# Kernel tuning notes

Hardware: AMD Instinct MI355X
Metric: run time of the kernel (lower is better)

## Reference

```python
import jax, jax.numpy as jnp
import numpy as np

D = 1024        # embedding_dim
H = 16          # num_heads
HKV = 4         # num_kv_heads
HD = D // H     # head_dim = 64
L = 64          # latent_dim
EPS = 1e-6
LN_EPS = 1e-5
B, S = 2, 1024


def _feat(x):
    # feature_map == 'elu': elu(x) + 1 (non-negative features)
    return jax.nn.elu(x) + 1.0


def setup_inputs() -> dict:
    key = jax.random.key(0)
    ks = jax.random.split(key, 8)
    w = lambda k, shape: (jax.random.normal(k, shape, jnp.float32) * 0.02)
    return {
        "x": jax.random.normal(ks[0], (B, S, D), jnp.float32),
        "Wq": w(ks[1], (D, D)), "bq": jnp.zeros((D,), jnp.float32),
        "Wk": w(ks[2], (D, HKV * HD)), "bk": jnp.zeros((HKV * HD,), jnp.float32),
        "Wv": w(ks[3], (D, HKV * HD)), "bv": jnp.zeros((HKV * HD,), jnp.float32),
        "Wc": w(ks[4], (HKV * HD, L)),   # kv_compress (no bias)
        "We": w(ks[5], (L, HKV * HD)),   # kv_expand (no bias)
        "Wo": w(ks[6], (D, D)), "bo": jnp.zeros((D,), jnp.float32),
        "gamma": jnp.ones((D,), jnp.float32),
        "beta": jnp.zeros((D,), jnp.float32),
    }


def reference(x, Wq, bq, Wk, bk, Wv, bv, Wc, We, Wo, bo, gamma, beta):
    b, s, _ = x.shape
    residual = x
    # projections
    q = x @ Wq + bq                     # [b,s,D]
    k = x @ Wk + bk                     # [b,s,HKV*HD]
    v = x @ Wv + bv
    # latent compress -> expand
    k = (k @ Wc) @ We                   # [b,s,HKV*HD]
    v = (v @ Wc) @ We
    # split heads
    q = q.reshape(b, s, H, HD).transpose(0, 2, 1, 3)      # [b,H,s,HD]
    k = k.reshape(b, s, HKV, HD).transpose(0, 2, 1, 3)    # [b,HKV,s,HD]
    v = v.reshape(b, s, HKV, HD).transpose(0, 2, 1, 3)
    # GQA: repeat KV heads per query group
    rep = H // HKV
    k = jnp.repeat(k, rep, axis=1)                        # [b,H,s,HD]
    v = jnp.repeat(v, rep, axis=1)
    # causal linear attention via cumulative KV outer-product state
    qf = _feat(q)                                          # [b,h,s,f]
    kf = _feat(k)
    kv = jnp.einsum('bhsf,bhsd->bhsfd', kf, v)             # [b,h,s,f,d]
    kv_cum = jnp.cumsum(kv, axis=2)
    num = jnp.einsum('bhsf,bhsfd->bhsd', qf, kv_cum)
    den = jnp.einsum('bhsf,bhsf->bhs', qf, jnp.cumsum(kf, axis=2))[..., None] + EPS
    o = num / den                                          # [b,h,s,d]
    # merge heads, output projection
    o = o.transpose(0, 2, 1, 3).reshape(b, s, D)
    o = o @ Wo + bo
    # residual + layernorm (epsilon=1e-5)
    y = residual + o
    mu = jnp.mean(y, axis=-1, keepdims=True)
    var = jnp.var(y, axis=-1, keepdims=True)
    return (y - mu) / jnp.sqrt(var + LN_EPS) * gamma + beta
```

## Files before the change

kernel.cpp:

```cpp
#include <hip/hip_runtime.h>

#define D_ 1024
#define H_ 16
#define HKV_ 4
#define B_ 2
#define S_ 1024
#define BS_ (B_*S_)
#define QKVW 1536
#define QB 64
#define NC (S_/QB)

typedef short bf8 __attribute__((ext_vector_type(8)));
typedef float f32x4 __attribute__((ext_vector_type(4)));

#define MFMA_B16(a,b,c) __builtin_amdgcn_mfma_f32_16x16x32_bf16((a),(b),(c),0,0,0)

#define GLOAD16(g, l) __builtin_amdgcn_global_load_lds( \
    (const __attribute__((address_space(1))) void*)(g), \
    (__attribute__((address_space(3))) void*)(l), 16, 0, 0)

#define SW(row, idx) ((idx) ^ (((row) & 7) << 3))

__device__ __forceinline__ unsigned short f2b(float f) {
  unsigned int u = __float_as_uint(f);
  u += 0x7FFFu + ((u >> 16) & 1u);
  return (unsigned short)(u >> 16);
}
__device__ __forceinline__ float b2f(unsigned short h) {
  return __uint_as_float(((unsigned int)h) << 16);
}
__device__ __forceinline__ float feat(float x) { return x > 0.f ? x + 1.f : __expf(x); }

__device__ __forceinline__ void conv_body(const float* __restrict__ src,
                                          unsigned short* __restrict__ dst,
                                          int sub, int n4, int tid) {
  int i = sub * 256 + tid;
  if (i >= n4) return;
  float4 v = ((const float4*)src)[i];
  ushort4 o;
  o.x = f2b(v.x); o.y = f2b(v.y); o.z = f2b(v.z); o.w = f2b(v.w);
  ((ushort4*)dst)[i] = o;
}

__device__ __forceinline__ void tconv_body(const float* __restrict__ src,
                                           unsigned short* __restrict__ dst,
                                           int bx, int by, int ss, int ds,
                                           int tid, float (*tl)[65]) {
  int r0 = by * 64, c0 = bx * 64;
  int ty = tid >> 4, tx4 = (tid & 15) * 4;
#pragma unroll
  for (int rep = 0; rep < 4; ++rep) {
    int r = ty + rep * 16;
    float4 v = *(const float4*)&src[(size_t)(r0 + r) * ss + c0 + tx4];
    tl[r][tx4] = v.x; tl[r][tx4 + 1] = v.y; tl[r][tx4 + 2] = v.z; tl[r][tx4 + 3] = v.w;
  }
  __syncthreads();
#pragma unroll
  for (int rep = 0; rep < 4; ++rep) {
    int c = ty + rep * 16;
    ushort4 o;
    o.x = f2b(tl[tx4 + 0][c]); o.y = f2b(tl[tx4 + 1][c]);
    o.z = f2b(tl[tx4 + 2][c]); o.w = f2b(tl[tx4 + 3][c]);
    *(ushort4*)&dst[(size_t)(c0 + c) * ds + r0 + tx4] = o;
  }
}

__global__ __launch_bounds__(256) void k_prep(const float* __restrict__ x,
                                              const float* __restrict__ Wq,
                                              const float* __restrict__ Wo,
                                              const float* __restrict__ Wk,
                                              const float* __restrict__ Wv,
                                              const float* __restrict__ Wc,
                                              const float* __restrict__ We,
                                              unsigned short* __restrict__ xb,
                                              unsigned short* __restrict__ Wqkv_t,
                                              unsigned short* __restrict__ Wo_t,
                                              unsigned short* __restrict__ Wkv_b,
                                              float* __restrict__ Wce,
                                              unsigned short* __restrict__ Wce_t) {
  __shared__ float tl[64][65];
  __shared__ __align__(16) unsigned short As[64][72];
  __shared__ __align__(16) unsigned short Bs[128][72];
  int blk = blockIdx.x, tid = threadIdx.x;
  if (blk < 2048) {
    conv_body(x, xb, blk, BS_ * D_ / 4, tid);
  } else if (blk < 2304) {
    conv_body(Wk, Wkv_b, blk - 2048, 1024 * 256 / 4, tid);
  } else if (blk < 2560) {
    conv_body(Wv, Wkv_b + 1024 * 256, blk - 2304, 1024 * 256 / 4, tid);
  } else if (blk < 2816) {
    int sb = blk - 2560;
    tconv_body(Wq, Wqkv_t, sb & 15, sb >> 4, 1024, 1024, tid, tl);
  } else if (blk < 3072) {
    int sb = blk - 2816;
    tconv_body(Wo, Wo_t, sb & 15, sb >> 4, 1024, 1024, tid, tl);
  } else {
    int sb = blk - 3072;
    int row0 = (sb >> 1) * 64, col0 = (sb & 1) * 128;
    {
      int r = tid >> 2, c0 = (tid & 3) * 16;
      const float* src = &Wc[(size_t)(row0 + r) * 64 + c0];
#pragma unroll
      for (int e = 0; e < 16; e += 4) {
        float4 v = *(const float4*)(src + e);
        As[r][c0 + e] = f2b(v.x); As[r][c0 + e + 1] = f2b(v.y);
        As[r][c0 + e + 2] = f2b(v.z); As[r][c0 + e + 3] = f2b(v.w);
      }
      int k = tid >> 2, cb = (tid & 3) * 32;
      const float* wsrc = &We[(size_t)k * 256 + col0 + cb];
#pragma unroll
      for (int e = 0; e < 32; e += 4) {
        float4 v = *(const float4*)(wsrc + e);
        Bs[cb + e][k] = f2b(v.x); Bs[cb + e + 1][k] = f2b(v.y);
        Bs[cb + e + 2][k] = f2b(v.z); Bs[cb + e + 3][k] = f2b(v.w);
      }
    }
    __syncthreads();
    const int lane = tid & 63, wave = tid >> 6;
    const int lr = lane & 15, lq = lane >> 4;
    const int wc0 = wave * 32;
    const f32x4 fzero = {0.f, 0.f, 0.f, 0.f};
    f32x4 acc[4][2];
#pragma unroll
    for (int i = 0; i < 4; ++i) { acc[i][0] = fzero; acc[i][1] = fzero; }
#pragma unroll
    for (int kk = 0; kk < 2; ++kk)
#pragma unroll
      for (int mi = 0; mi < 4; ++mi) {
        bf8 a = *(const bf8*)&As[mi * 16 + lr][kk * 32 + lq * 8];
#pragma unroll
        for (int ni = 0; ni < 2; ++ni) {
          bf8 bb = *(const bf8*)&Bs[wc0 + ni * 16 + lr][kk * 32 + lq * 8];
          acc[mi][ni] = MFMA_B16(a, bb, acc[mi][ni]);
        }
      }
#pragma unroll
    for (int mi = 0; mi < 4; ++mi)
#pragma unroll
      for (int ni = 0; ni < 2; ++ni) {
        int col = col0 + wc0 + ni * 16 + lr;
#pragma unroll
        for (int r = 0; r < 4; ++r) {
          int row = row0 + mi * 16 + lq * 4 + r;
          float v = acc[mi][ni][r];
          Wce[(size_t)row * 256 + col] = v;
          Wce_t[(size_t)col * 256 + row] = f2b(v);
        }
      }
  }
}

template<int MODE>
__global__ __launch_bounds__(64) void k_gemm1(const unsigned short* __restrict__ A,
                                              const unsigned short* __restrict__ Bt,
                                              const float* __restrict__ bias,
                                              unsigned short* __restrict__ C,
                                              int N, int K) {
  __shared__ __align__(16) unsigned short As[2][64 * 64];
  __shared__ __align__(16) unsigned short Bs[2][64 * 64];
  const int lane = threadIdx.x;
  const int row0 = blockIdx.y * 64, col0 = blockIdx.x * 64;
  const int lr = lane & 15, lq = lane >> 4;
  const int rsub = lane >> 3, sj = lane & 7;
  const int js = sj ^ rsub;
  const f32x4 fzero = {0.f, 0.f, 0.f, 0.f};
  f32x4 acc[4][4];
#pragma unroll
  for (int i = 0; i < 4; ++i)
#pragma unroll
    for (int j = 0; j < 4; ++j) acc[i][j] = fzero;

#define STAGE64(pb, k0)                                                        \
  {                                                                            \
    _Pragma("unroll")                                                          \
    for (int i = 0; i < 8; ++i)                                                \
      GLOAD16(&A[(size_t)(row0 + i * 8 + rsub) * K + (k0) + js * 8],           \
              &As[pb][(i * 512 + lane * 8)]);                                  \
    _Pragma("unroll")                                                          \
    for (int i = 0; i < 8; ++i)                                                \
      GLOAD16(&Bt[(size_t)(col0 + i * 8 + rsub) * K + (k0) + js * 8],          \
              &Bs[pb][(i * 512 + lane * 8)]);                                  \
  }

  STAGE64(0, 0);
  int cur = 0;
  for (int k0 = 0; k0 < K; k0 += 64) {
    if (k0 + 64 < K) {
      STAGE64(cur ^ 1, k0 + 64);
      asm volatile("s_waitcnt vmcnt(16)" ::: "memory");
    } else {
      asm volatile("s_waitcnt vmcnt(0)" ::: "memory");
    }
    __builtin_amdgcn_sched_barrier(0);
    bf8 af[2][4], bfr[2][4];
#pragma unroll
    for (int kk = 0; kk < 2; ++kk)
#pragma unroll
      for (int mi = 0; mi < 4; ++mi) {
        int ch = (kk * 4 + lq) ^ (lr & 7);
        af[kk][mi]  = *(const bf8*)&As[cur][(mi * 16 + lr) * 64 + ch * 8];
        bfr[kk][mi] = *(const bf8*)&Bs[cur][(mi * 16 + lr) * 64 + ch * 8];
      }
#pragma unroll
    for (int kk = 0; kk < 2; ++kk)
#pragma unroll
      for (int mi = 0; mi < 4; ++mi)
#pragma unroll
        for (int ni = 0; ni < 4; ++ni)
          acc[mi][ni] = MFMA_B16(af[kk][mi], bfr[kk][ni], acc[mi][ni]);
    cur ^= 1;
  }
#undef STAGE64
#pragma unroll
  for (int ni = 0; ni < 4; ++ni) {
    int col = col0 + ni * 16 + lr;
    float bv = bias[col];
#pragma unroll
    for (int mi = 0; mi < 4; ++mi)
#pragma unroll
      for (int r = 0; r < 4; ++r) {
        int row = row0 + mi * 16 + lq * 4 + r;
        float v = acc[mi][ni][r] + bv;
        if (MODE == 1 && col < 1280) v = feat(v);
        C[(size_t)row * N + col] = f2b(v);
      }
  }
}

__global__ __launch_bounds__(128) void k_fold(const unsigned short* __restrict__ A,
                                              const unsigned short* __restrict__ Bt,
                                              unsigned short* __restrict__ C,
                                              float* __restrict__ biasq,
                                              int N, int K,
                                              const float* __restrict__ fbq,
                                              const float* __restrict__ fbk,
                                              const float* __restrict__ fbv,
                                              const float* __restrict__ fWce) {
  if (blockIdx.y == 4) {
    int t = blockIdx.x * 128 + threadIdx.x;
    if (t >= QKVW) return;
    if (t < 1024) { biasq[t] = fbq[t]; return; }
    const float* b = (t < 1280) ? fbk : fbv;
    int n = (t < 1280) ? (t - 1024) : (t - 1280);
    float s = 0.f;
    for (int j = 0; j < 256; ++j) s += b[j] * fWce[j * 256 + n];
    biasq[t] = s;
    return;
  }
  __shared__ __align__(16) unsigned short As[64 * 32];
  __shared__ __align__(16) unsigned short Bs[128 * 32];
  const int tid = threadIdx.x;
  const int lane = tid & 63, wave = tid >> 6;
  const int row0 = blockIdx.y * 64, col0 = blockIdx.x * 128;
  const f32x4 fzero = {0.f, 0.f, 0.f, 0.f};
  f32x4 acc[4][4];
#pragma unroll
  for (int i = 0; i < 4; ++i)
#pragma unroll
    for (int j = 0; j < 4; ++j) acc[i][j] = fzero;
  const int lr = lane & 15, lq = lane >> 4, lk = lq * 8;
  for (int k0 = 0; k0 < K; k0 += 32) {
#pragma unroll
    for (int i = 0; i < 2; ++i) {
      int e = (tid + i * 128) * 8;
      int r = e >> 5, c = e & 31;
      GLOAD16(&A[(size_t)(row0 + r) * K + k0 + c], &As[e]);
    }
#pragma unroll
    for (int i = 0; i < 4; ++i) {
      int e = (tid + i * 128) * 8;
      int r = e >> 5, c = e & 31;
      GLOAD16(&Bt[(size_t)(col0 + r) * K + k0 + c], &Bs[e]);
    }
    __syncthreads();
    bf8 af[4], bfr[4];
#pragma unroll
    for (int mi = 0; mi < 4; ++mi)
      af[mi] = *(const bf8*)&As[(mi * 16 + lr) * 32 + lk];
#pragma unroll
    for (int ni = 0; ni < 4; ++ni)
      bfr[ni] = *(const bf8*)&Bs[(wave * 64 + ni * 16 + lr) * 32 + lk];
#pragma unroll
    for (int mi = 0; mi < 4; ++mi)
#pragma unroll
      for (int ni = 0; ni < 4; ++ni)
        acc[mi][ni] = MFMA_B16(af[mi], bfr[ni], acc[mi][ni]);
    __syncthreads();
  }
#pragma unroll
  for (int mi = 0; mi < 4; ++mi)
#pragma unroll
    for (int ni = 0; ni < 4; ++ni) {
      int col = col0 + wave * 64 + ni * 16 + lr;
#pragma unroll
      for (int r = 0; r < 4; ++r) {
        int row = row0 + mi * 16 + lq * 4 + r;
        int sec = col >> 10, cc = col & 1023;
        C[(size_t)(1024 + sec * 256 + row) * 1024 + cc] = f2b(acc[mi][ni][r]);
      }
    }
}

__global__ __launch_bounds__(256) void k_vkv(const unsigned short* __restrict__ qkvb,
                                             unsigned short* __restrict__ vt,
                                             float* __restrict__ stc) {
  __shared__ unsigned short tl[64][72];
  __shared__ float Kf[64 * 64];
  int c = blockIdx.x, g = blockIdx.y, b = blockIdx.z;
  int tid = threadIdx.x;
  int s0 = c * QB;
  {
    int j = tid >> 2, f0 = (tid & 3) * 16;
    const unsigned short* kr = &qkvb[(size_t)(b * S_ + s0 + j) * QKVW + 1024 + g * 64 + f0];
    const unsigned short* vr = &qkvb[(size_t)(b * S_ + s0 + j) * QKVW + 1280 + g * 64 + f0];
    uint4 k0_ = *(const uint4*)kr;
    uint4 k1_ = *(const uint4*)(kr + 8);
    const unsigned short* ks = (const unsigned short*)&k0_;
#pragma unroll
    for (int e = 0; e < 8; ++e) Kf[j * 64 + f0 + e] = b2f(ks[e]);
    ks = (const unsigned short*)&k1_;
#pragma unroll
    for (int e = 0; e < 8; ++e) Kf[j * 64 + f0 + 8 + e] = b2f(ks[e]);
    *(uint4*)&tl[j][f0] = *(const uint4*)vr;
    *(uint4*)&tl[j][f0 + 8] = *(const uint4*)(vr + 8);
  }
  __syncthreads();
  {
    int ty = tid >> 4, tx4 = (tid & 15) * 4;
#pragma unroll
    for (int rep = 0; rep < 4; ++rep) {
      int d = ty + rep * 16;
      ushort4 o;
      o.x = tl[tx4 + 0][d]; o.y = tl[tx4 + 1][d];
      o.z = tl[tx4 + 2][d]; o.w = tl[tx4 + 3][d];
      *(ushort4*)&vt[((size_t)(b * HKV_ + g) * 64 + d) * S_ + s0 + tx4] = o;
    }
  }
  int d = tid >> 2, f0 = (tid & 3) * 16;
  float acc[16];
#pragma unroll
  for (int e = 0; e < 16; ++e) acc[e] = 0.f;
#pragma unroll 4
  for (int j = 0; j < QB; ++j) {
    float vv = b2f(tl[j][d]);
    const float* kfr = &Kf[j * 64 + f0];
#pragma unroll
    for (int e = 0; e < 16; ++e) acc[e] += vv * kfr[e];
  }
  size_t base = ((size_t)((b * HKV_ + g) * NC + c) * 65 + d) * 64 + f0;
#pragma unroll
  for (int e = 0; e < 16; ++e) stc[base + e] = acc[e];
  if (tid < 64) {
    float z = 0.f;
    for (int j = 0; j < QB; ++j) z += Kf[j * 64 + tid];
    stc[((size_t)((b * HKV_ + g) * NC + c) * 65 + 64) * 64 + tid] = z;
  }
}

__global__ __launch_bounds__(256) void k_scan(const float* __restrict__ stc,
                                              unsigned short* __restrict__ stp,
                                              float* __restrict__ zp) {
  int t = blockIdx.x * 256 + threadIdx.x;
  if (t >= 8 * 65 * 64) return;
  int bg = t / (65 * 64);
  int e = t - bg * (65 * 64);
  int d = e >> 6, f = e & 63;
  float run = 0.f;
#pragma unroll
  for (int c = 0; c < NC; ++c) {
    if (d < 64) stp[(size_t)(bg * NC + c) * 4096 + e] = f2b(run);
    else        zp[(bg * NC + c) * 64 + f] = run;
    run += stc[((size_t)(bg * NC + c) * 65 + d) * 64 + f];
  }
}

__global__ __launch_bounds__(512) void k_attn(const unsigned short* __restrict__ qkvb,
                                              const unsigned short* __restrict__ vt,
                                              const unsigned short* __restrict__ stp,
                                              const float* __restrict__ zp,
                                              unsigned short* __restrict__ ob) {
  __shared__ __align__(16) unsigned short Qf[2][64 * 64];
  __shared__ __align__(16) unsigned short Kf[64 * 64];
  __shared__ __align__(16) unsigned short Vl[64 * 64];
  __shared__ __align__(16) unsigned short Sl[64 * 64];
  __shared__ __align__(16) unsigned short P[2][64 * 64];
  __shared__ __align__(16) unsigned short Ol[64][144];
  __shared__ float zl[64];
  __shared__ float den[2][64];
  int c = blockIdx.x, hp = blockIdx.y, b = blockIdx.z;
  int g = hp >> 1;
  int tid = threadIdx.x, lane = tid & 63, wave = tid >> 6;
  int s0 = c * QB;
  {
    int hsel = tid >> 8, t = tid & 255;
    int j = t >> 2, f0 = (t & 3) * 16;
    const unsigned short* qr =
        &qkvb[(size_t)(b * S_ + s0 + j) * QKVW + (hp * 2 + hsel) * 64 + f0];
    *(uint4*)&Qf[hsel][SW(j, j * 64 + f0)]     = *(const uint4*)qr;
    *(uint4*)&Qf[hsel][SW(j, j * 64 + f0 + 8)] = *(const uint4*)(qr + 8);
    if (tid < 256) {
      const unsigned short* kr =
          &qkvb[(size_t)(b * S_ + s0 + j) * QKVW + 1024 + g * 64 + f0];
      *(uint4*)&Kf[SW(j, j * 64 + f0)]     = *(const uint4*)kr;
      *(uint4*)&Kf[SW(j, j * 64 + f0 + 8)] = *(const uint4*)(kr + 8);
    } else {
      const unsigned short* vbase = &vt[((size_t)(b * HKV_ + g) * 64) * S_ + s0];
#pragma unroll
      for (int i2 = 0; i2 < 2; ++i2) {
        int cc = t * 2 + i2;
        int dd = cc >> 3, col = (cc & 7) * 8;
        *(uint4*)&Vl[SW(dd, cc * 8)] = *(const uint4*)&vbase[(size_t)dd * S_ + col];
      }
    }
    const unsigned short* sbase = &stp[(size_t)((b * HKV_ + g) * NC + c) * 4096];
    { int dd = tid >> 3; *(uint4*)&Sl[SW(dd, tid * 8)] = *(const uint4*)&sbase[tid * 8]; }
    if (tid < 64) zl[tid] = zp[((b * HKV_ + g) * NC + c) * 64 + tid];
  }
  __syncthreads();
  const int lr = lane & 15, lq = lane >> 4, lk = lq * 8;
  const int hh = wave >> 2, rw = (wave & 3) * 16;
  const f32x4 fzero = {0.f, 0.f, 0.f, 0.f};
  bf8 aQ[2];
#pragma unroll
  for (int kk = 0; kk < 2; ++kk)
    aQ[kk] = *(const bf8*)&Qf[hh][SW(rw + lr, (rw + lr) * 64 + kk * 32 + lk)];
  f32x4 sc[4];
#pragma unroll
  for (int nj = 0; nj < 4; ++nj) sc[nj] = fzero;
#pragma unroll
  for (int nj = 0; nj < 4; ++nj)
#pragma unroll
    for (int kk = 0; kk < 2; ++kk) {
      bf8 bk8 = *(const bf8*)&Kf[SW(nj * 16 + lr, (nj * 16 + lr) * 64 + kk * 32 + lk)];
      sc[nj] = MFMA_B16(aQ[kk], bk8, sc[nj]);
    }
#pragma unroll
  for (int nj = 0; nj < 4; ++nj)
#pragma unroll
    for (int r = 0; r < 4; ++r) {
      int i = rw + lq * 4 + r;
      int j = nj * 16 + lr;
      float v = (j <= i) ? sc[nj][r] : 0.f;
      P[hh][SW(i, i * 64 + j)] = f2b(v);
    }
  __syncthreads();
  {
    int hd = tid >> 8, t = tid & 255;
    int i = t >> 2, q = t & 3, f0 = q * 16;
    float s = 0.f;
#pragma unroll
    for (int e = 0; e < 16; ++e) s += b2f(P[hd][SW(i, i * 64 + f0 + e)]);
#pragma unroll
    for (int e = 0; e < 16; ++e) s += b2f(Qf[hd][SW(i, i * 64 + f0 + e)]) * zl[f0 + e];
    s += __shfl_xor(s, 1);
    s += __shfl_xor(s, 2);
    if (q == 0) den[hd][i] = s;
  }
  f32x4 oa[4];
#pragma unroll
  for (int nd = 0; nd < 4; ++nd) oa[nd] = fzero;
  bf8 aP[2];
#pragma unroll
  for (int kk = 0; kk < 2; ++kk)
    aP[kk] = *(const bf8*)&P[hh][SW(rw + lr, (rw + lr) * 64 + kk * 32 + lk)];
#pragma unroll
  for (int nd = 0; nd < 4; ++nd)
#pragma unroll
    for (int kk = 0; kk < 2; ++kk) {
      bf8 bS = *(const bf8*)&Sl[SW(nd * 16 + lr, (nd * 16 + lr) * 64 + kk * 32 + lk)];
      oa[nd] = MFMA_B16(aQ[kk], bS, oa[nd]);
      bf8 bV = *(const bf8*)&Vl[SW(nd * 16 + lr, (nd * 16 + lr) * 64 + kk * 32 + lk)];
      oa[nd] = MFMA_B16(aP[kk], bV, oa[nd]);
    }
  __syncthreads();
#pragma unroll
  for (int nd = 0; nd < 4; ++nd)
#pragma unroll
    for (int r = 0; r < 4; ++r) {
      int i = rw + lq * 4 + r;
      int dd = nd * 16 + lr;
      Ol[i][hh * 64 + dd] = f2b(oa[nd][r] / (den[hh][i] + 1e-6f));
    }
  __syncthreads();
  {
    int j = tid >> 3, u = tid & 7;
    unsigned short* orow = &ob[(size_t)(b * S_ + s0 + j) * D_ + hp * 128 + u * 16];
    *(uint4*)orow       = *(const uint4*)&Ol[j][u * 16];
    *(uint4*)(orow + 8) = *(const uint4*)&Ol[j][u * 16 + 8];
  }
}

__global__ __launch_bounds__(256) void k_ln(const unsigned short* __restrict__ xb,
                                            const unsigned short* __restrict__ o2,
                                            const float* __restrict__ gamma,
                                            const float* __restrict__ beta,
                                            float* __restrict__ out) {
  int row = blockIdx.x, tid = threadIdx.x;
  ushort4 xv = ((const ushort4*)(xb + (size_t)row * D_))[tid];
  ushort4 ov = ((const ushort4*)(o2 + (size_t)row * D_))[tid];
  float4 y;
  y.x = b2f(xv.x) + b2f(ov.x); y.y = b2f(xv.y) + b2f(ov.y);
  y.z = b2f(xv.z) + b2f(ov.z); y.w = b2f(xv.w) + b2f(ov.w);
  float s = y.x + y.y + y.z + y.w;
  float ss = y.x * y.x + y.y * y.y + y.z * y.z + y.w * y.w;
#pragma unroll
  for (int off = 32; off > 0; off >>= 1) {
    s += __shfl_down(s, off);
    ss += __shfl_down(ss, off);
  }
  __shared__ float red[8];
  int lane = tid & 63, wave = tid >> 6;
  if (lane == 0) { red[wave] = s; red[4 + wave] = ss; }
  __syncthreads();
  if (tid == 0) {
    red[0] = red[0] + red[1] + red[2] + red[3];
    red[4] = red[4] + red[5] + red[6] + red[7];
  }
  __syncthreads();
  float mu = red[0] * (1.f / D_);
  float var = red[4] * (1.f / D_) - mu * mu;
  float rs = rsqrtf(var + 1e-5f);
  float4 g4 = ((const float4*)gamma)[tid];
  float4 b4 = ((const float4*)beta)[tid];
  float4 o;
  o.x = (y.x - mu) * rs * g4.x + b4.x;
  o.y = (y.y - mu) * rs * g4.y + b4.y;
  o.z = (y.z - mu) * rs * g4.z + b4.z;
  o.w = (y.w - mu) * rs * g4.w + b4.w;
  ((float4*)(out + (size_t)row * D_))[tid] = o;
}

extern "C" void kernel_launch(void* const* d_in, const int* in_sizes, int n_in,
                              void* d_out, int out_size, void* d_ws, size_t ws_size,
                              hipStream_t stream) {
  const float* x     = (const float*)d_in[0];
  const float* Wq    = (const float*)d_in[1];
  const float* bq    = (const float*)d_in[2];
  const float* Wk    = (const float*)d_in[3];
  const float* bk    = (const float*)d_in[4];
  const float* Wv    = (const float*)d_in[5];
  const float* bv    = (const float*)d_in[6];
  const float* Wc    = (const float*)d_in[7];
  const float* We    = (const float*)d_in[8];
  const float* Wo    = (const float*)d_in[9];
  const float* bo    = (const float*)d_in[10];
  const float* gamma = (const float*)d_in[11];
  const float* beta  = (const float*)d_in[12];

  char* p = (char*)d_ws;
  size_t off = 0;
  auto carve = [&](size_t bytes) {
    void* r = p + off;
    off = (off + bytes + 255) & ~(size_t)255;
    return r;
  };
  unsigned short* xb     = (unsigned short*)carve((size_t)BS_ * D_ * 2);
  unsigned short* Wqkv_t = (unsigned short*)carve((size_t)QKVW * D_ * 2);
  unsigned short* Wo_t   = (unsigned short*)carve((size_t)D_ * D_ * 2);
  float*          biasq  = (float*)carve(QKVW * 4);
  unsigned short* qkvb   = (unsigned short*)carve((size_t)BS_ * QKVW * 2);
  float*          Wce    = (float*)carve(256 * 256 * 4);
  unsigned short* Wce_t  = (unsigned short*)carve(256 * 256 * 2);
  unsigned short* Wkv_b  = (unsigned short*)carve((size_t)2048 * 256 * 2);
  unsigned short* vtb    = (unsigned short*)carve((size_t)8 * 64 * S_ * 2);
  float*          stc    = (float*)carve((size_t)8 * NC * 65 * 64 * 4);
  unsigned short* stp    = (unsigned short*)carve((size_t)8 * NC * 4096 * 2);
  float*          zp     = (float*)carve((size_t)8 * NC * 64 * 4);
  unsigned short* obuf   = (unsigned short*)carve((size_t)BS_ * D_ * 2);
  unsigned short* o2     = (unsigned short*)carve((size_t)BS_ * D_ * 2);

  k_prep<<<3080, 256, 0, stream>>>(x, Wq, Wo, Wk, Wv, Wc, We,
                                   xb, Wqkv_t, Wo_t, Wkv_b, Wce, Wce_t);
  k_fold<<<dim3(16, 5), 128, 0, stream>>>(Wce_t, Wkv_b, Wqkv_t, biasq,
                                          2048, 256, bq, bk, bv, Wce);
  k_gemm1<1><<<dim3(24, 32), 64, 0, stream>>>(xb, Wqkv_t, biasq, qkvb, QKVW, 1024);
  k_vkv<<<dim3(NC, HKV_, B_), 256, 0, stream>>>(qkvb, vtb, stc);
  k_scan<<<(8 * 65 * 64 + 255) / 256, 256, 0, stream>>>(stc, stp, zp);
  k_attn<<<dim3(NC, H_ / 2, B_), 512, 0, stream>>>(qkvb, vtb, stp, zp, obuf);
  k_gemm1<0><<<dim3(16, 32), 64, 0, stream>>>(obuf, Wo_t, bo, o2, 1024, 1024);
  k_ln<<<BS_, 256, 0, stream>>>(xb, o2, gamma, beta, (float*)d_out);
}
```

Before: 90.92 us.

## Fuse chunk state, scan and attention into one cooperative kernel

Merges the per-chunk KV state kernel, the prefix scan kernel and the attention kernel into a single cooperative launch of 256 blocks, using grid-wide syncs between phases. V is loaded directly from the QKV buffer and transposed in shared memory, so the separate V-transpose buffer is dropped. This removes two kernel launches and a global round trip for V, at the cost of two grid barriers and a scan phase that runs on only 65 of the 256 blocks.

```diff
diff --git a/kernel.cpp b/kernel.cpp
--- a/kernel.cpp
+++ b/kernel.cpp
@@ -1,4 +1,7 @@
 #include <hip/hip_runtime.h>
+#include <hip/hip_cooperative_groups.h>
+
+namespace cg = cooperative_groups;
 
 #define D_ 1024
 #define H_ 16
@@ -301,84 +304,12 @@
     }
 }
 
-__global__ __launch_bounds__(256) void k_vkv(const unsigned short* __restrict__ qkvb,
-                                             unsigned short* __restrict__ vt,
-                                             float* __restrict__ stc) {
-  __shared__ unsigned short tl[64][72];
-  __shared__ float Kf[64 * 64];
-  int c = blockIdx.x, g = blockIdx.y, b = blockIdx.z;
-  int tid = threadIdx.x;
-  int s0 = c * QB;
-  {
-    int j = tid >> 2, f0 = (tid & 3) * 16;
-    const unsigned short* kr = &qkvb[(size_t)(b * S_ + s0 + j) * QKVW + 1024 + g * 64 + f0];
-    const unsigned short* vr = &qkvb[(size_t)(b * S_ + s0 + j) * QKVW + 1280 + g * 64 + f0];
-    uint4 k0_ = *(const uint4*)kr;
-    uint4 k1_ = *(const uint4*)(kr + 8);
-    const unsigned short* ks = (const unsigned short*)&k0_;
-#pragma unroll
-    for (int e = 0; e < 8; ++e) Kf[j * 64 + f0 + e] = b2f(ks[e]);
-    ks = (const unsigned short*)&k1_;
-#pragma unroll
-    for (int e = 0; e < 8; ++e) Kf[j * 64 + f0 + 8 + e] = b2f(ks[e]);
-    *(uint4*)&tl[j][f0] = *(const uint4*)vr;
-    *(uint4*)&tl[j][f0 + 8] = *(const uint4*)(vr + 8);
-  }
-  __syncthreads();
-  {
-    int ty = tid >> 4, tx4 = (tid & 15) * 4;
-#pragma unroll
-    for (int rep = 0; rep < 4; ++rep) {
-      int d = ty + rep * 16;
-      ushort4 o;
-      o.x = tl[tx4 + 0][d]; o.y = tl[tx4 + 1][d];
-      o.z = tl[tx4 + 2][d]; o.w = tl[tx4 + 3][d];
-      *(ushort4*)&vt[((size_t)(b * HKV_ + g) * 64 + d) * S_ + s0 + tx4] = o;
-    }
-  }
-  int d = tid >> 2, f0 = (tid & 3) * 16;
-  float acc[16];
-#pragma unroll
-  for (int e = 0; e < 16; ++e) acc[e] = 0.f;
-#pragma unroll 4
-  for (int j = 0; j < QB; ++j) {
-    float vv = b2f(tl[j][d]);
-    const float* kfr = &Kf[j * 64 + f0];
-#pragma unroll
-    for (int e = 0; e < 16; ++e) acc[e] += vv * kfr[e];
-  }
-  size_t base = ((size_t)((b * HKV_ + g) * NC + c) * 65 + d) * 64 + f0;
-#pragma unroll
-  for (int e = 0; e < 16; ++e) stc[base + e] = acc[e];
-  if (tid < 64) {
-    float z = 0.f;
-    for (int j = 0; j < QB; ++j) z += Kf[j * 64 + tid];
-    stc[((size_t)((b * HKV_ + g) * NC + c) * 65 + 64) * 64 + tid] = z;
-  }
-}
-
-__global__ __launch_bounds__(256) void k_scan(const float* __restrict__ stc,
-                                              unsigned short* __restrict__ stp,
-                                              float* __restrict__ zp) {
-  int t = blockIdx.x * 256 + threadIdx.x;
-  if (t >= 8 * 65 * 64) return;
-  int bg = t / (65 * 64);
-  int e = t - bg * (65 * 64);
-  int d = e >> 6, f = e & 63;
-  float run = 0.f;
-#pragma unroll
-  for (int c = 0; c < NC; ++c) {
-    if (d < 64) stp[(size_t)(bg * NC + c) * 4096 + e] = f2b(run);
-    else        zp[(bg * NC + c) * 64 + f] = run;
-    run += stc[((size_t)(bg * NC + c) * 65 + d) * 64 + f];
-  }
-}
-
-__global__ __launch_bounds__(512) void k_attn(const unsigned short* __restrict__ qkvb,
-                                              const unsigned short* __restrict__ vt,
-                                              const unsigned short* __restrict__ stp,
-                                              const float* __restrict__ zp,
-                                              unsigned short* __restrict__ ob) {
+__global__ __launch_bounds__(512) void k_fused(const unsigned short* __restrict__ qkvb,
+                                               float* __restrict__ stc,
+                                               unsigned short* __restrict__ stp,
+                                               float* __restrict__ zp,
+                                               unsigned short* __restrict__ ob) {
+  cg::grid_group gg = cg::this_grid();
   __shared__ __align__(16) unsigned short Qf[2][64 * 64];
   __shared__ __align__(16) unsigned short Kf[64 * 64];
   __shared__ __align__(16) unsigned short Vl[64 * 64];
@@ -387,7 +318,8 @@
   __shared__ __align__(16) unsigned short Ol[64][144];
   __shared__ float zl[64];
   __shared__ float den[2][64];
-  int c = blockIdx.x, hp = blockIdx.y, b = blockIdx.z;
+  int bid = blockIdx.x;
+  int c = bid & 15, hp = (bid >> 4) & 7, b = bid >> 7;
   int g = hp >> 1;
   int tid = threadIdx.x, lane = tid & 63, wave = tid >> 6;
   int s0 = c * QB;
@@ -404,16 +336,60 @@
       *(uint4*)&Kf[SW(j, j * 64 + f0)]     = *(const uint4*)kr;
       *(uint4*)&Kf[SW(j, j * 64 + f0 + 8)] = *(const uint4*)(kr + 8);
     } else {
-      const unsigned short* vbase = &vt[((size_t)(b * HKV_ + g) * 64) * S_ + s0];
-#pragma unroll
-      for (int i2 = 0; i2 < 2; ++i2) {
-        int cc = t * 2 + i2;
-        int dd = cc >> 3, col = (cc & 7) * 8;
-        *(uint4*)&Vl[SW(dd, cc * 8)] = *(const uint4*)&vbase[(size_t)dd * S_ + col];
-      }
-    }
+      const unsigned short* vr =
+          &qkvb[(size_t)(b * S_ + s0 + j) * QKVW + 1280 + g * 64 + f0];
+      *(uint4*)&Ol[j][f0]     = *(const uint4*)vr;
+      *(uint4*)&Ol[j][f0 + 8] = *(const uint4*)(vr + 8);
+    }
+  }
+  __syncthreads();
+  {
+    int d = tid >> 3, sq = (tid & 7) * 8;
+    unsigned short tmp[8];
+#pragma unroll
+    for (int e = 0; e < 8; ++e) tmp[e] = Ol[sq + e][d];
+    *(uint4*)&Vl[SW(d, d * 64 + sq)] = *(const uint4*)tmp;
+  }
+  __syncthreads();
+  if ((hp & 1) == 0) {
+    int d = tid >> 3, f0 = (tid & 7) * 8;
+    float acc[8];
+#pragma unroll
+    for (int e = 0; e < 8; ++e) acc[e] = 0.f;
+    for (int s = 0; s < 64; ++s) {
+      float vv = b2f(Vl[SW(d, d * 64 + s)]);
+      int kb = SW(s, s * 64 + f0);
+#pragma unroll
+      for (int e = 0; e < 8; ++e) acc[e] += vv * b2f(Kf[kb + e]);
+    }
+    size_t base = ((size_t)((b * HKV_ + g) * NC + c) * 65 + d) * 64 + f0;
+#pragma unroll
+    for (int e = 0; e < 8; ++e) stc[base + e] = acc[e];
+    if (tid < 64) {
+      float z = 0.f;
+      for (int s = 0; s < 64; ++s) z += b2f(Kf[SW(s, s * 64 + tid)]);
+      stc[((size_t)((b * HKV_ + g) * NC + c) * 65 + 64) * 64 + tid] = z;
+    }
+  }
+  gg.sync();
+  if (bid < 65) {
+    int t = bid * 512 + tid;
+    int bg = t / (65 * 64);
+    int e = t - bg * (65 * 64);
+    int d = e >> 6, f = e & 63;
+    float run = 0.f;
+#pragma unroll
+    for (int cc = 0; cc < NC; ++cc) {
+      if (d < 64) stp[(size_t)(bg * NC + cc) * 4096 + e] = f2b(run);
+      else        zp[(bg * NC + cc) * 64 + f] = run;
+      run += stc[((size_t)(bg * NC + cc) * 65 + d) * 64 + f];
+    }
+  }
+  gg.sync();
+  {
     const unsigned short* sbase = &stp[(size_t)((b * HKV_ + g) * NC + c) * 4096];
-    { int dd = tid >> 3; *(uint4*)&Sl[SW(dd, tid * 8)] = *(const uint4*)&sbase[tid * 8]; }
+    int dd = tid >> 3;
+    *(uint4*)&Sl[SW(dd, tid * 8)] = *(const uint4*)&sbase[tid * 8];
     if (tid < 64) zl[tid] = zp[((b * HKV_ + g) * NC + c) * 64 + tid];
   }
   __syncthreads();
@@ -562,7 +538,6 @@
   float*          Wce    = (float*)carve(256 * 256 * 4);
   unsigned short* Wce_t  = (unsigned short*)carve(256 * 256 * 2);
   unsigned short* Wkv_b  = (unsigned short*)carve((size_t)2048 * 256 * 2);
-  unsigned short* vtb    = (unsigned short*)carve((size_t)8 * 64 * S_ * 2);
   float*          stc    = (float*)carve((size_t)8 * NC * 65 * 64 * 4);
   unsigned short* stp    = (unsigned short*)carve((size_t)8 * NC * 4096 * 2);
   float*          zp     = (float*)carve((size_t)8 * NC * 64 * 4);
@@ -574,9 +549,11 @@
   k_fold<<<dim3(16, 5), 128, 0, stream>>>(Wce_t, Wkv_b, Wqkv_t, biasq,
                                           2048, 256, bq, bk, bv, Wce);
   k_gemm1<1><<<dim3(24, 32), 64, 0, stream>>>(xb, Wqkv_t, biasq, qkvb, QKVW, 1024);
-  k_vkv<<<dim3(NC, HKV_, B_), 256, 0, stream>>>(qkvb, vtb, stc);
-  k_scan<<<(8 * 65 * 64 + 255) / 256, 256, 0, stream>>>(stc, stp, zp);
-  k_attn<<<dim3(NC, H_ / 2, B_), 512, 0, stream>>>(qkvb, vtb, stp, zp, obuf);
+  {
+    void* args[] = {(void*)&qkvb, (void*)&stc, (void*)&stp, (void*)&zp, (void*)&obuf};
+    hipLaunchCooperativeKernel((const void*)k_fused, dim3(256), dim3(512),
+                               args, 0, stream);
+  }
   k_gemm1<0><<<dim3(16, 32), 64, 0, stream>>>(obuf, Wo_t, bo, o2, 1024, 1024);
   k_ln<<<BS_, 256, 0, stream>>>(xb, o2, gamma, beta, (float*)d_out);
 }
```

Result: slower. 150.6 us (+65.6%).

## Fold chunk-state prefix scan and V transpose into attention kernel

Applied to the files above, without the earlier changes.

Removes the separate k_scan kernel and the global V-transpose buffer. Each attention block now sums the per-chunk KV states and normaliser vectors of all earlier chunks directly from stc. It also loads V rows from the QKV buffer and transposes them in shared memory. This saves a launch and several global round trips, but repeats the prefix sum across blocks and heads, so later chunks do up to 15 extra reads and adds per block.

```diff
diff --git a/kernel.cpp b/kernel.cpp
--- a/kernel.cpp
+++ b/kernel.cpp
@@ -302,7 +302,6 @@
 }
 
 __global__ __launch_bounds__(256) void k_vkv(const unsigned short* __restrict__ qkvb,
-                                             unsigned short* __restrict__ vt,
                                              float* __restrict__ stc) {
   __shared__ unsigned short tl[64][72];
   __shared__ float Kf[64 * 64];
@@ -325,17 +324,6 @@
     *(uint4*)&tl[j][f0 + 8] = *(const uint4*)(vr + 8);
   }
   __syncthreads();
-  {
-    int ty = tid >> 4, tx4 = (tid & 15) * 4;
-#pragma unroll
-    for (int rep = 0; rep < 4; ++rep) {
-      int d = ty + rep * 16;
-      ushort4 o;
-      o.x = tl[tx4 + 0][d]; o.y = tl[tx4 + 1][d];
-      o.z = tl[tx4 + 2][d]; o.w = tl[tx4 + 3][d];
-      *(ushort4*)&vt[((size_t)(b * HKV_ + g) * 64 + d) * S_ + s0 + tx4] = o;
-    }
-  }
   int d = tid >> 2, f0 = (tid & 3) * 16;
   float acc[16];
 #pragma unroll
@@ -357,27 +345,8 @@
   }
 }
 
-__global__ __launch_bounds__(256) void k_scan(const float* __restrict__ stc,
-                                              unsigned short* __restrict__ stp,
-                                              float* __restrict__ zp) {
-  int t = blockIdx.x * 256 + threadIdx.x;
-  if (t >= 8 * 65 * 64) return;
-  int bg = t / (65 * 64);
-  int e = t - bg * (65 * 64);
-  int d = e >> 6, f = e & 63;
-  float run = 0.f;
-#pragma unroll
-  for (int c = 0; c < NC; ++c) {
-    if (d < 64) stp[(size_t)(bg * NC + c) * 4096 + e] = f2b(run);
-    else        zp[(bg * NC + c) * 64 + f] = run;
-    run += stc[((size_t)(bg * NC + c) * 65 + d) * 64 + f];
-  }
-}
-
 __global__ __launch_bounds__(512) void k_attn(const unsigned short* __restrict__ qkvb,
-                                              const unsigned short* __restrict__ vt,
-                                              const unsigned short* __restrict__ stp,
-                                              const float* __restrict__ zp,
+                                              const float* __restrict__ stc,
                                               unsigned short* __restrict__ ob) {
   __shared__ __align__(16) unsigned short Qf[2][64 * 64];
   __shared__ __align__(16) unsigned short Kf[64 * 64];
@@ -404,17 +373,68 @@
       *(uint4*)&Kf[SW(j, j * 64 + f0)]     = *(const uint4*)kr;
       *(uint4*)&Kf[SW(j, j * 64 + f0 + 8)] = *(const uint4*)(kr + 8);
     } else {
-      const unsigned short* vbase = &vt[((size_t)(b * HKV_ + g) * 64) * S_ + s0];
-#pragma unroll
-      for (int i2 = 0; i2 < 2; ++i2) {
-        int cc = t * 2 + i2;
-        int dd = cc >> 3, col = (cc & 7) * 8;
-        *(uint4*)&Vl[SW(dd, cc * 8)] = *(const uint4*)&vbase[(size_t)dd * S_ + col];
-      }
-    }
-    const unsigned short* sbase = &stp[(size_t)((b * HKV_ + g) * NC + c) * 4096];
-    { int dd = tid >> 3; *(uint4*)&Sl[SW(dd, tid * 8)] = *(const uint4*)&sbase[tid * 8]; }
-    if (tid < 64) zl[tid] = zp[((b * HKV_ + g) * NC + c) * 64 + tid];
+      const unsigned short* vr =
+          &qkvb[(size_t)(b * S_ + s0 + j) * QKVW + 1280 + g * 64 + f0];
+      *(uint4*)&Ol[j][f0]     = *(const uint4*)vr;
+      *(uint4*)&Ol[j][f0 + 8] = *(const uint4*)(vr + 8);
+    }
+  }
+  __syncthreads();
+  {
+    int d = tid >> 3, sq = (tid & 7) * 8;
+    unsigned short tmp[8];
+#pragma unroll
+    for (int e = 0; e < 8; ++e) tmp[e] = Ol[sq + e][d];
+    *(uint4*)&Vl[SW(d, d * 64 + sq)] = *(const uint4*)tmp;
+  }
+  {
+    int dd = tid >> 3, col = (tid & 7) * 8;
+    const float* sb = stc + (size_t)(b * HKV_ + g) * NC * 4160 + dd * 64 + col;
+    float p0[8], p1[8], p2[8], p3[8];
+#pragma unroll
+    for (int e = 0; e < 8; ++e) { p0[e] = 0.f; p1[e] = 0.f; p2[e] = 0.f; p3[e] = 0.f; }
+    int cc = 0;
+    for (; cc + 4 <= c; cc += 4) {
+      const float* q0 = sb + (size_t)(cc + 0) * 4160;
+      const float* q1 = sb + (size_t)(cc + 1) * 4160;
+      const float* q2 = sb + (size_t)(cc + 2) * 4160;
+      const float* q3 = sb + (size_t)(cc + 3) * 4160;
+      float4 a0 = *(const float4*)q0, b0 = *(const float4*)(q0 + 4);
+      float4 a1 = *(const float4*)q1, b1 = *(const float4*)(q1 + 4);
+      float4 a2 = *(const float4*)q2, b2 = *(const float4*)(q2 + 4);
+      float4 a3 = *(const float4*)q3, b3 = *(const float4*)(q3 + 4);
+      p0[0] += a0.x; p0[1] += a0.y; p0[2] += a0.z; p0[3] += a0.w;
+      p0[4] += b0.x; p0[5] += b0.y; p0[6] += b0.z; p0[7] += b0.w;
+      p1[0] += a1.x; p1[1] += a1.y; p1[2] += a1.z; p1[3] += a1.w;
+      p1[4] += b1.x; p1[5] += b1.y; p1[6] += b1.z; p1[7] += b1.w;
+      p2[0] += a2.x; p2[1] += a2.y; p2[2] += a2.z; p2[3] += a2.w;
+      p2[4] += b2.x; p2[5] += b2.y; p2[6] += b2.z; p2[7] += b2.w;
+      p3[0] += a3.x; p3[1] += a3.y; p3[2] += a3.z; p3[3] += a3.w;
+      p3[4] += b3.x; p3[5] += b3.y; p3[6] += b3.z; p3[7] += b3.w;
+    }
+    for (; cc < c; ++cc) {
+      const float* q0 = sb + (size_t)cc * 4160;
+      float4 a0 = *(const float4*)q0, b0 = *(const float4*)(q0 + 4);
+      p0[0] += a0.x; p0[1] += a0.y; p0[2] += a0.z; p0[3] += a0.w;
+      p0[4] += b0.x; p0[5] += b0.y; p0[6] += b0.z; p0[7] += b0.w;
+    }
+    unsigned short o[8];
+#pragma unroll
+    for (int e = 0; e < 8; ++e) o[e] = f2b(p0[e] + p1[e] + p2[e] + p3[e]);
+    *(uint4*)&Sl[SW(dd, dd * 64 + col)] = *(const uint4*)o;
+    if (tid < 64) {
+      const float* zb = stc + (size_t)(b * HKV_ + g) * NC * 4160 + 64 * 64 + tid;
+      float z0 = 0.f, z1 = 0.f, z2 = 0.f, z3 = 0.f;
+      int c2 = 0;
+      for (; c2 + 4 <= c; c2 += 4) {
+        z0 += zb[(size_t)(c2 + 0) * 4160];
+        z1 += zb[(size_t)(c2 + 1) * 4160];
+        z2 += zb[(size_t)(c2 + 2) * 4160];
+        z3 += zb[(size_t)(c2 + 3) * 4160];
+      }
+      for (; c2 < c; ++c2) z0 += zb[(size_t)c2 * 4160];
+      zl[tid] = z0 + z1 + z2 + z3;
+    }
   }
   __syncthreads();
   const int lr = lane & 15, lq = lane >> 4, lk = lq * 8;
@@ -562,10 +582,7 @@
   float*          Wce    = (float*)carve(256 * 256 * 4);
   unsigned short* Wce_t  = (unsigned short*)carve(256 * 256 * 2);
   unsigned short* Wkv_b  = (unsigned short*)carve((size_t)2048 * 256 * 2);
-  unsigned short* vtb    = (unsigned short*)carve((size_t)8 * 64 * S_ * 2);
   float*          stc    = (float*)carve((size_t)8 * NC * 65 * 64 * 4);
-  unsigned short* stp    = (unsigned short*)carve((size_t)8 * NC * 4096 * 2);
-  float*          zp     = (float*)carve((size_t)8 * NC * 64 * 4);
   unsigned short* obuf   = (unsigned short*)carve((size_t)BS_ * D_ * 2);
   unsigned short* o2     = (unsigned short*)carve((size_t)BS_ * D_ * 2);
 
@@ -574,9 +591,8 @@
   k_fold<<<dim3(16, 5), 128, 0, stream>>>(Wce_t, Wkv_b, Wqkv_t, biasq,
                                           2048, 256, bq, bk, bv, Wce);
   k_gemm1<1><<<dim3(24, 32), 64, 0, stream>>>(xb, Wqkv_t, biasq, qkvb, QKVW, 1024);
-  k_vkv<<<dim3(NC, HKV_, B_), 256, 0, stream>>>(qkvb, vtb, stc);
-  k_scan<<<(8 * 65 * 64 + 255) / 256, 256, 0, stream>>>(stc, stp, zp);
-  k_attn<<<dim3(NC, H_ / 2, B_), 512, 0, stream>>>(qkvb, vtb, stp, zp, obuf);
+  k_vkv<<<dim3(NC, HKV_, B_), 256, 0, stream>>>(qkvb, stc);
+  k_attn<<<dim3(NC, H_ / 2, B_), 512, 0, stream>>>(qkvb, stc, obuf);
   k_gemm1<0><<<dim3(16, 32), 64, 0, stream>>>(obuf, Wo_t, bo, o2, 1024, 1024);
   k_ln<<<BS_, 256, 0, stream>>>(xb, o2, gamma, beta, (float*)d_out);
 }
```

Result: faster. 87.58 us (-3.7%).
